# Kernel optimization log

Measured on AMD Instinct MI355X. Metric: run time of the kernel, lower is better.

## Reference

```python
import jax, jax.numpy as jnp
import numpy as np

N_EXPERTS = 64
TOPK = 4
DIM = 2048
B_T = 8192


def setup_inputs() -> dict:
    key = jax.random.key(0)
    k1, k2 = jax.random.split(key)
    x = jax.random.normal(k1, (B_T, DIM), jnp.float32)
    W = jax.random.normal(k2, (N_EXPERTS, DIM), jnp.float32) * 0.02  # nn.Linear weight (out, in)
    router_bias = jnp.zeros((N_EXPERTS,), jnp.float32)  # registered buffer, init zeros
    return {"x": x, "W": W, "router_bias": router_bias, "token_capacity": 3072}


def _route(x, W, router_bias, token_capacity):
    """Faithful serial greedy capacity-aware routing.

    Replicates the torch nested loop (k-major, token-minor order):
      - per step, pick argmax over the token's (mutated) logits among experts
        with remaining capacity;
      - full experts whose logit exceeds the chosen one get permanently set
        to -inf in that token's logit row (exactly what the inner while-style
        loop does);
      - if no expert has capacity, selected stays -1, weight 0, and the whole
        row becomes -inf (torch sets the top expert to -inf n_experts times).
    """
    logits0 = x @ W.T + router_bias                       # (N, E)
    scores = jax.nn.softmax(logits0, axis=-1)             # (N, E)
    cap = token_capacity // TOPK                          # python int
    remaining0 = jnp.full((N_EXPERTS,), float(cap), jnp.float32)
    N = x.shape[0]
    NEG = jnp.float32(-jnp.inf)

    def step(carry, i):
        logits, remaining = carry
        b = i % N                                         # token index (k-major order)
        row = logits[b]                                   # (E,)
        masked = jnp.where(remaining > 0, row, NEG)
        chosen = jnp.argmax(masked)
        ok = remaining[chosen] > 0                        # False only if all experts full
        sel = jnp.where(ok, chosen, -1).astype(jnp.int32)
        w = jnp.where(ok, scores[b, chosen], jnp.float32(0.0))
        full = remaining <= 0
        cval = row[chosen]
        # full experts 'above' the chosen one were visited and zapped to -inf
        new_row = jnp.where(ok,
                            jnp.where(full & (row > cval), NEG, row),
                            jnp.full_like(row, NEG))
        logits = logits.at[b].set(new_row)
        remaining = remaining.at[chosen].add(jnp.where(ok, jnp.float32(-1.0), jnp.float32(0.0)))
        return (logits, remaining), (sel, w)

    (_, _), (sel_f, w_f) = jax.lax.scan(step, (logits0, remaining0),
                                        jnp.arange(TOPK * N))
    selected = sel_f.reshape(TOPK, N).T                   # (N, TOPK)
    weights = w_f.reshape(TOPK, N).T                      # (N, TOPK)
    weights = weights / (weights.sum(axis=-1, keepdims=True) + 1e-8)
    return selected, weights


def reference(x, W, router_bias, token_capacity):
    return _route(x, W, router_bias, token_capacity)
```

## Files before the change

### kernel.cpp

```cpp
#include <hip/hip_runtime.h>
#include <math.h>

#define N_TOK 8192
#define DIM   2048
#define NE    64
#define TOPK  4
#define THETA 2e-3f
#define TPB   64
#define NSPL  4
#define NSTRIP (N_TOK / TPB)
#define NBLK2 (NSTRIP * NSPL)
#define HSTR  16

typedef short bf16x8 __attribute__((ext_vector_type(8)));
typedef float f32x4  __attribute__((ext_vector_type(4)));

#define OFF_LOGITS 0
#define OFF_P      (OFF_LOGITS + N_TOK * NE)
#define OFF_MAXV   (OFF_P + NSPL * N_TOK * NE)
#define OFF_DENOM  (OFF_MAXV + N_TOK)
#define OFF_HIST   (OFF_DENOM + N_TOK)
#define OFF_WH     (OFF_HIST + NE * HSTR)
#define OFF_WL     (OFF_WH + NE * DIM / 2)
#define OFF_WT     (OFF_WL + NE * DIM / 2)
#define OFF_WTMP   (OFF_WT + NE * DIM)

__device__ inline void cvt2(float a, float b, unsigned& hi, unsigned& lo) {
    const unsigned ua = __float_as_uint(a), ub = __float_as_uint(b);
    hi = __builtin_amdgcn_perm(ub, ua, 0x07060302u);
    const float ra = a - __uint_as_float(ua & 0xFFFF0000u);
    const float rb = b - __uint_as_float(ub & 0xFFFF0000u);
    lo = __builtin_amdgcn_perm(__float_as_uint(rb), __float_as_uint(ra), 0x07060302u);
}

union FragU { unsigned u[4]; bf16x8 v; uint4 q; };

__device__ inline void make_frags(const float4& p, const float4& q,
                                  bf16x8& hi, bf16x8& lo) {
    FragU H, L;
    cvt2(p.x, p.y, H.u[0], L.u[0]);
    cvt2(p.z, p.w, H.u[1], L.u[1]);
    cvt2(q.x, q.y, H.u[2], L.u[2]);
    cvt2(q.z, q.w, H.u[3], L.u[3]);
    hi = H.v; lo = L.v;
}

__global__ __launch_bounds__(256)
void k_wc(const float* __restrict__ W, unsigned short* __restrict__ wh2,
          unsigned short* __restrict__ wl2, float* __restrict__ wt,
          int* __restrict__ hist) {
    const int t = blockIdx.x * 256 + threadIdx.x;
    if (t < NE * HSTR) hist[t] = 0;
    const int l  = t & 63;
    const int grp = t >> 6;
    const int nt = grp & 3;
    const int kc = grp >> 2;
    const int e  = nt * 16 + (l & 15);
    const int k0 = kc * 32 + (l >> 4) * 8;

    const float4 p = *reinterpret_cast<const float4*>(W + (size_t)e * DIM + k0);
    const float4 q = *reinterpret_cast<const float4*>(W + (size_t)e * DIM + k0 + 4);
    FragU H, L;
    cvt2(p.x, p.y, H.u[0], L.u[0]);
    cvt2(p.z, p.w, H.u[1], L.u[1]);
    cvt2(q.x, q.y, H.u[2], L.u[2]);
    cvt2(q.z, q.w, H.u[3], L.u[3]);
    const size_t off = (size_t)grp * 512 + l * 8;
    *reinterpret_cast<uint4*>(wh2 + off) = H.q;
    *reinterpret_cast<uint4*>(wl2 + off) = L.q;

    wt[(size_t)(k0 + 0) * NE + e] = p.x;
    wt[(size_t)(k0 + 1) * NE + e] = p.y;
    wt[(size_t)(k0 + 2) * NE + e] = p.z;
    wt[(size_t)(k0 + 3) * NE + e] = p.w;
    wt[(size_t)(k0 + 4) * NE + e] = q.x;
    wt[(size_t)(k0 + 5) * NE + e] = q.y;
    wt[(size_t)(k0 + 6) * NE + e] = q.z;
    wt[(size_t)(k0 + 7) * NE + e] = q.w;
}

__global__ __launch_bounds__(512, 4)
void k_main(const float* __restrict__ x, const unsigned short* __restrict__ wh2,
            const unsigned short* __restrict__ wl2, float* __restrict__ P) {
    __shared__ __align__(16) char smem[65536];

    const int tid   = threadIdx.x;
    const int ww    = tid >> 6;
    const int l     = tid & 63;
    const int strip = blockIdx.x >> 2;
    const int kq    = blockIdx.x & 3;
    const int t0    = strip * TPB;
    const int m     = l & 15;
    const int g     = l >> 4;
    const int tg    = ww >> 1;
    const int eg    = ww & 1;

    f32x4 accA[2], accB[2];
    #pragma unroll
    for (int n = 0; n < 2; ++n)
        #pragma unroll
        for (int r = 0; r < 4; ++r) { accA[n][r] = 0.0f; accB[n][r] = 0.0f; }

    const int arow = tg * 16 + m;
    const int axor = arow & 15;

    for (int win = 0; win < 4; ++win) {
        const int wk = kq * 4 + win;
        #pragma unroll
        for (int j = 0; j < 8; ++j) {
            const int dbase = ww * 8192 + j * 1024;
            const int d = dbase + l * 16;
            const char* src;
            if (dbase < 32768) {
                const int r = d >> 9;
                const int p = (d >> 4) & 31;
                const int s = p ^ (r & 15);
                src = (const char*)(x + (size_t)(t0 + r) * DIM
                                    + wk * 128 + s * 4);
            } else if (dbase < 49152) {
                src = (const char*)wh2 + (size_t)wk * 16384 + (d - 32768);
            } else {
                src = (const char*)wl2 + (size_t)wk * 16384 + (d - 49152);
            }
            __builtin_amdgcn_global_load_lds(
                (const __attribute__((address_space(1))) void*)src,
                (__attribute__((address_space(3))) void*)(smem + dbase),
                16, 0, 0);
        }
        asm volatile("s_waitcnt vmcnt(0)" ::: "memory");
        __syncthreads();

        const char* A = smem + arow * 512;
        #pragma unroll
        for (int kc = 0; kc < 4; ++kc) {
            const int s0 = kc * 8 + g * 2;
            const float4 pf = *reinterpret_cast<const float4*>(A + ((s0 ^ axor) << 4));
            const float4 qf = *reinterpret_cast<const float4*>(A + (((s0 + 1) ^ axor) << 4));
            bf16x8 ah, al;
            make_frags(pf, qf, ah, al);
            #pragma unroll
            for (int n = 0; n < 2; ++n) {
                const int nt = eg * 2 + n;
                FragU bh_, bl_;
                bh_.q = *reinterpret_cast<const uint4*>(smem + 32768 + (kc * 4 + nt) * 1024 + l * 16);
                bl_.q = *reinterpret_cast<const uint4*>(smem + 49152 + (kc * 4 + nt) * 1024 + l * 16);
                accA[n] = __builtin_amdgcn_mfma_f32_16x16x32_bf16(ah, bh_.v, accA[n], 0, 0, 0);
                accB[n] = __builtin_amdgcn_mfma_f32_16x16x32_bf16(al, bh_.v, accB[n], 0, 0, 0);
                accB[n] = __builtin_amdgcn_mfma_f32_16x16x32_bf16(ah, bl_.v, accB[n], 0, 0, 0);
            }
        }
        __syncthreads();
    }

    float* dst = P + (size_t)kq * N_TOK * NE;
    #pragma unroll
    for (int n = 0; n < 2; ++n)
        #pragma unroll
        for (int r = 0; r < 4; ++r)
            dst[(size_t)(t0 + tg * 16 + g * 4 + r) * NE + eg * 32 + n * 16 + m] =
                accA[n][r] + accB[n][r];
}

__global__ __launch_bounds__(256)
void k_reduce(const float* __restrict__ P, const float* __restrict__ bias,
              const float* __restrict__ x, const float* __restrict__ wt,
              float* __restrict__ logits, float* __restrict__ maxv,
              float* __restrict__ denomv, int* __restrict__ hist,
              float* __restrict__ out) {
    __shared__ float lbuf[32][68];
    __shared__ float part[4][68];
    __shared__ int   selS[32];
    __shared__ float wS[32];
    __shared__ short flagIdx[32];
    __shared__ int   flagCnt;

    const int tid = threadIdx.x;
    const int ww  = tid >> 6;
    const int l   = tid & 63;
    const int t0  = blockIdx.x * 32;

    if (tid == 0) flagCnt = 0;

    for (int q = tid; q < 32 * 16; q += 256) {
        const int t = q >> 4, e4 = (q & 15) << 2;
        const size_t idx = (size_t)(t0 + t) * NE + e4;
        float4 s = *reinterpret_cast<const float4*>(P + idx);
        const float4 b1 = *reinterpret_cast<const float4*>(P + (size_t)N_TOK * NE + idx);
        const float4 b2 = *reinterpret_cast<const float4*>(P + (size_t)2 * N_TOK * NE + idx);
        const float4 b3 = *reinterpret_cast<const float4*>(P + (size_t)3 * N_TOK * NE + idx);
        const float4 bb = *reinterpret_cast<const float4*>(bias + e4);
        s.x += b1.x + b2.x + b3.x + bb.x;
        s.y += b1.y + b2.y + b3.y + bb.y;
        s.z += b1.z + b2.z + b3.z + bb.z;
        s.w += b1.w + b2.w + b3.w + bb.w;
        *reinterpret_cast<float4*>(logits + idx) = s;
        *reinterpret_cast<float4*>(&lbuf[t][e4]) = s;
    }
    __syncthreads();

    #pragma unroll
    for (int tt = 0; tt < 8; ++tt) {
        const int t = ww * 8 + tt;
        const float lv = lbuf[t][l];
        float v1 = lv; int i1 = l; float v2 = -INFINITY;
        #pragma unroll
        for (int off = 32; off; off >>= 1) {
            const float ov1 = __shfl_xor(v1, off);
            const int   oi1 = __shfl_xor(i1, off);
            const float ov2 = __shfl_xor(v2, off);
            if (ov1 > v1 || (ov1 == v1 && oi1 < i1)) {
                v2 = fmaxf(v1, ov2); v1 = ov1; i1 = oi1;
            } else {
                v2 = fmaxf(v2, ov1);
            }
        }
        float s = expf(lv - v1);
        #pragma unroll
        for (int off = 32; off; off >>= 1) s += __shfl_xor(s, off);
        if (l == 0) {
            const int row = t0 + t;
            maxv[row]   = v1;
            denomv[row] = s;
            selS[t]     = i1;
            wS[t]       = 1.0f / s;
            if (v1 - v2 < THETA) {
                const int ix = atomicAdd(&flagCnt, 1);
                flagIdx[ix] = (short)t;
            }
        }
    }
    __syncthreads();

    const int nf = flagCnt;
    for (int fi = 0; fi < nf; ++fi) {
        const int tl  = flagIdx[fi];
        const int row = t0 + tl;
        const float* xr = x + (size_t)row * DIM + ww * 512;
        const float* wb = wt + (size_t)(ww * 512) * NE + l;
        float a0 = 0.0f, a1 = 0.0f;
        #pragma unroll 4
        for (int k = 0; k < 512; k += 8) {
            const float4 x0 = *reinterpret_cast<const float4*>(xr + k);
            const float4 x1 = *reinterpret_cast<const float4*>(xr + k + 4);
            a0 = fmaf(x0.x, wb[(size_t)(k + 0) * NE], a0);
            a0 = fmaf(x0.y, wb[(size_t)(k + 1) * NE], a0);
            a0 = fmaf(x0.z, wb[(size_t)(k + 2) * NE], a0);
            a0 = fmaf(x0.w, wb[(size_t)(k + 3) * NE], a0);
            a1 = fmaf(x1.x, wb[(size_t)(k + 4) * NE], a1);
            a1 = fmaf(x1.y, wb[(size_t)(k + 5) * NE], a1);
            a1 = fmaf(x1.z, wb[(size_t)(k + 6) * NE], a1);
            a1 = fmaf(x1.w, wb[(size_t)(k + 7) * NE], a1);
        }
        part[ww][l] = a0 + a1;
        __syncthreads();
        if (ww == 0) {
            float lg = bias[l];
            #pragma unroll
            for (int s2 = 0; s2 < 4; ++s2) lg += part[s2][l];
            logits[(size_t)row * NE + l] = lg;
            float v = lg; int idx = l;
            #pragma unroll
            for (int off = 32; off; off >>= 1) {
                const float ov = __shfl_xor(v, off);
                const int   oi = __shfl_xor(idx, off);
                if (ov > v || (ov == v && oi < idx)) { v = ov; idx = oi; }
            }
            float p = expf(lg - v);
            #pragma unroll
            for (int off = 32; off; off >>= 1) p += __shfl_xor(p, off);
            if (l == 0) {
                maxv[row]   = v;
                denomv[row] = p;
                selS[tl]    = idx;
                wS[tl]      = 1.0f / p;
            }
        }
        __syncthreads();
    }

    if (ww == 0) {
        int cnt = 0;
        #pragma unroll
        for (int t = 0; t < 32; ++t) cnt += (selS[t] == l) ? 1 : 0;
        if (cnt) atomicAdd(&hist[l * HSTR], cnt);
    }

    if (tid < 32) {
        const int row = t0 + tid;
        const float se = (float)selS[tid];
        const float wv = wS[tid];
        const float wn = wv / (4.0f * wv + 1e-8f);
        *reinterpret_cast<float4*>(out + (size_t)row * 4) = make_float4(se, se, se, se);
        *reinterpret_cast<float4*>(out + (size_t)N_TOK * TOPK + (size_t)row * 4) =
            make_float4(wn, wn, wn, wn);
    }
}

__global__ __launch_bounds__(256)
void k_decide(const int* __restrict__ hist, const float* __restrict__ logits,
              const float* __restrict__ maxv, const float* __restrict__ denomv,
              const int* __restrict__ tc, float* __restrict__ out,
              float* __restrict__ wtmp) {
    __shared__ int flagS;
    const int tid = threadIdx.x;
    const int cap = tc[0] / TOPK;
    if (tid < NE) {
        const bool bad = (TOPK * hist[tid * HSTR] > cap);
        const unsigned long long mm = __ballot(bad);
        if (tid == 0) flagS = (mm == 0ull) ? 1 : 0;
    }
    __syncthreads();
    if (flagS) return;

    if (tid < 64) {
        const int e = tid;
        int rem = cap;
        for (int k = 0; k < TOPK; ++k) {
            for (int b = 0; b < N_TOK; ++b) {
                const float lg = logits[(size_t)b * NE + e];
                float v = (rem > 0) ? lg : -INFINITY;
                int idx = e;
                #pragma unroll
                for (int off = 32; off; off >>= 1) {
                    const float ov = __shfl_xor(v, off);
                    const int   oi = __shfl_xor(idx, off);
                    if (ov > v || (ov == v && oi < idx)) { v = ov; idx = oi; }
                }
                const bool ok = (v != -INFINITY);
                if (ok && e == idx) rem -= 1;
                const float lc = __shfl(lg, idx);
                if (e == 0) {
                    out[(size_t)b * TOPK + k]  = ok ? (float)idx : -1.0f;
                    wtmp[(size_t)b * TOPK + k] = ok ? expf(lc - maxv[b]) / denomv[b] : 0.0f;
                }
            }
        }
    }
    __syncthreads();
    for (int b = tid; b < N_TOK; b += 256) {
        const float w0 = wtmp[b * 4 + 0], w1_ = wtmp[b * 4 + 1];
        const float w2 = wtmp[b * 4 + 2], w3 = wtmp[b * 4 + 3];
        const float s = ((w0 + w1_) + w2) + w3 + 1e-8f;
        out[N_TOK * TOPK + b * 4 + 0] = w0 / s;
        out[N_TOK * TOPK + b * 4 + 1] = w1_ / s;
        out[N_TOK * TOPK + b * 4 + 2] = w2 / s;
        out[N_TOK * TOPK + b * 4 + 3] = w3 / s;
    }
}

extern "C" void kernel_launch(void* const* d_in, const int* in_sizes, int n_in,
                              void* d_out, int out_size, void* d_ws, size_t ws_size,
                              hipStream_t stream) {
    const float* x    = (const float*)d_in[0];
    const float* W    = (const float*)d_in[1];
    const float* bias = (const float*)d_in[2];
    const int*   tc   = (const int*)d_in[3];

    float* ws       = (float*)d_ws;
    float* logits   = ws + OFF_LOGITS;
    float* Pp       = ws + OFF_P;
    float* maxv     = ws + OFF_MAXV;
    float* denomv   = ws + OFF_DENOM;
    int*   hist     = (int*)(ws + OFF_HIST);
    unsigned short* wh2 = (unsigned short*)(ws + OFF_WH);
    unsigned short* wl2 = (unsigned short*)(ws + OFF_WL);
    float* wt       = ws + OFF_WT;
    float* wtmp     = ws + OFF_WTMP;
    float* out      = (float*)d_out;

    k_wc<<<NE * DIM / 8 / 256, 256, 0, stream>>>(W, wh2, wl2, wt, hist);
    k_main<<<NBLK2, 512, 0, stream>>>(x, wh2, wl2, Pp);
    k_reduce<<<N_TOK / 32, 256, 0, stream>>>(Pp, bias, x, wt, logits, maxv,
                                             denomv, hist, out);
    k_decide<<<1, 256, 0, stream>>>(hist, logits, maxv, denomv, tc, out, wtmp);
}
```

Before: 153.1 us.

## Add low-low bf16 MFMA term, tighten tie threshold, vectorize fp32 recompute

New measurement: 148.2 us. -3.2%, faster.

```diff
diff --git a/kernel.cpp b/kernel.cpp
--- a/kernel.cpp
+++ b/kernel.cpp
@@ -5,7 +5,7 @@
 #define DIM   2048
 #define NE    64
 #define TOPK  4
-#define THETA 2e-3f
+#define THETA 2e-4f
 #define TPB   64
 #define NSPL  4
 #define NSTRIP (N_TOK / TPB)
@@ -147,6 +147,7 @@
                 accA[n] = __builtin_amdgcn_mfma_f32_16x16x32_bf16(ah, bh_.v, accA[n], 0, 0, 0);
                 accB[n] = __builtin_amdgcn_mfma_f32_16x16x32_bf16(al, bh_.v, accB[n], 0, 0, 0);
                 accB[n] = __builtin_amdgcn_mfma_f32_16x16x32_bf16(ah, bl_.v, accB[n], 0, 0, 0);
+                accB[n] = __builtin_amdgcn_mfma_f32_16x16x32_bf16(al, bl_.v, accB[n], 0, 0, 0);
             }
         }
         __syncthreads();
@@ -169,6 +170,7 @@
               float* __restrict__ out) {
     __shared__ float lbuf[32][68];
     __shared__ float part[4][68];
+    __shared__ float xs[DIM];
     __shared__ int   selS[32];
     __shared__ float wS[32];
     __shared__ short flagIdx[32];
@@ -235,23 +237,33 @@
     for (int fi = 0; fi < nf; ++fi) {
         const int tl  = flagIdx[fi];
         const int row = t0 + tl;
-        const float* xr = x + (size_t)row * DIM + ww * 512;
-        const float* wb = wt + (size_t)(ww * 512) * NE + l;
-        float a0 = 0.0f, a1 = 0.0f;
-        #pragma unroll 4
-        for (int k = 0; k < 512; k += 8) {
-            const float4 x0 = *reinterpret_cast<const float4*>(xr + k);
-            const float4 x1 = *reinterpret_cast<const float4*>(xr + k + 4);
-            a0 = fmaf(x0.x, wb[(size_t)(k + 0) * NE], a0);
-            a0 = fmaf(x0.y, wb[(size_t)(k + 1) * NE], a0);
-            a0 = fmaf(x0.z, wb[(size_t)(k + 2) * NE], a0);
-            a0 = fmaf(x0.w, wb[(size_t)(k + 3) * NE], a0);
-            a1 = fmaf(x1.x, wb[(size_t)(k + 4) * NE], a1);
-            a1 = fmaf(x1.y, wb[(size_t)(k + 5) * NE], a1);
-            a1 = fmaf(x1.z, wb[(size_t)(k + 6) * NE], a1);
-            a1 = fmaf(x1.w, wb[(size_t)(k + 7) * NE], a1);
-        }
-        part[ww][l] = a0 + a1;
+        for (int j = tid; j < DIM / 4; j += 256)
+            *reinterpret_cast<float4*>(&xs[j * 4]) =
+                *reinterpret_cast<const float4*>(x + (size_t)row * DIM + j * 4);
+        __syncthreads();
+
+        const int eq = l & 15;
+        const int kg = l >> 4;
+        const float4* wt4 = reinterpret_cast<const float4*>(wt);
+        float4 acc = make_float4(0.f, 0.f, 0.f, 0.f);
+        #pragma unroll 8
+        for (int i = 0; i < 128; ++i) {
+            const int k = ww * 512 + i * 4 + kg;
+            const float4 wq = wt4[(size_t)k * 16 + eq];
+            const float xv = xs[k];
+            acc.x = fmaf(xv, wq.x, acc.x);
+            acc.y = fmaf(xv, wq.y, acc.y);
+            acc.z = fmaf(xv, wq.z, acc.z);
+            acc.w = fmaf(xv, wq.w, acc.w);
+        }
+        #pragma unroll
+        for (int off = 16; off <= 32; off <<= 1) {
+            acc.x += __shfl_xor(acc.x, off);
+            acc.y += __shfl_xor(acc.y, off);
+            acc.z += __shfl_xor(acc.z, off);
+            acc.w += __shfl_xor(acc.w, off);
+        }
+        if (l < 16) *reinterpret_cast<float4*>(&part[ww][l * 4]) = acc;
         __syncthreads();
         if (ww == 0) {
             float lg = bias[l];
```
